# Performance work log

Measured on AMD Instinct MI355X. Metric: run time of the kernel, lower is better.

Reference implementation:

```python
import jax, jax.numpy as jnp
import numpy as np

LN_EPS = 1e-5

def setup_inputs() -> dict:
    key = jax.random.key(0)
    ks = jax.random.split(key, 4)
    B, N, D, De = 4, 2048, 128, 8
    h = jax.random.normal(ks[0], (B, N, D), dtype=jnp.float32)
    e = jax.random.normal(ks[1], (B, N, N, De), dtype=jnp.float32)
    W_w = jax.random.normal(ks[2], (D, D), dtype=jnp.float32) * (1.0 / np.sqrt(D))
    W_b = jax.random.normal(ks[3], (D,), dtype=jnp.float32) * 0.02
    ln_g = jnp.ones((D,), dtype=jnp.float32)
    ln_b = jnp.zeros((D,), dtype=jnp.float32)
    return {"h": h, "e": e, "W_w": W_w, "W_b": W_b, "ln_g": ln_g, "ln_b": ln_b}

def _layernorm(x, g, b):
    mu = jnp.mean(x, axis=-1, keepdims=True)
    var = jnp.var(x, axis=-1, keepdims=True)
    return (x - mu) * jax.lax.rsqrt(var + LN_EPS) * g + b

def reference(h, e, W_w, W_b, ln_g, ln_b):
    # w_ij = softmax_j(||e_ij||)  -> [B, N, N]
    scores = jnp.linalg.norm(e, axis=-1)          # [B, N, N]
    w = jax.nn.softmax(scores, axis=2)            # softmax over neighbor dim j
    # agg_i = sum_j w_ij * h_j  (batched matmul instead of O(B N^2 D) broadcast)
    agg = jnp.einsum('bij,bjd->bid', w, h)        # [B, N, D]
    z = (h + agg) @ W_w.T + W_b                   # Linear
    h_new = jax.nn.relu(_layernorm(z, ln_g, ln_b)) + h
    return (h_new, e)
```

## Files before the change

kernel.cpp:

```cpp
#include <hip/hip_runtime.h>
#include <hip/hip_bf16.h>
#include <math.h>

constexpr int B  = 4;
constexpr int N  = 2048;
constexpr int D  = 128;
constexpr int De = 8;
constexpr int KS = 8;
constexpr float LN_EPS = 1e-5f;

__device__ inline ushort f2bf(float f) {
    uint u = __float_as_uint(f);
    return (ushort)((u + 0x7fffu + ((u >> 16) & 1u)) >> 16);
}

__global__ __launch_bounds__(256) void k_escore(const float* __restrict__ e,
                                                float* __restrict__ out_e,
                                                ushort* __restrict__ w16,
                                                long long total) {
    long long stride = (long long)gridDim.x * blockDim.x;
    for (long long idx = (long long)blockIdx.x * blockDim.x + threadIdx.x;
         idx < total; idx += stride) {
        const float4* src = reinterpret_cast<const float4*>(e + idx * De);
        float4 a  = src[0];
        float4 b4 = src[1];
        float4* dst = reinterpret_cast<float4*>(out_e + idx * De);
        dst[0] = a;
        dst[1] = b4;
        float ss = a.x * a.x + a.y * a.y + a.z * a.z + a.w * a.w
                 + b4.x * b4.x + b4.y * b4.y + b4.z * b4.z + b4.w * b4.w;
        w16[idx] = f2bf(__expf(sqrtf(ss)));
    }
}

__global__ __launch_bounds__(256) void k_rowsum(const ushort* __restrict__ w16,
                                                float* __restrict__ inv_rowsum) {
    __shared__ float red[4];
    long long row = blockIdx.x;
    int t = threadIdx.x;
    uint4 v = *reinterpret_cast<const uint4*>(w16 + row * (long long)N + t * 8);
    uint u[4] = {v.x, v.y, v.z, v.w};
    float s = 0.0f;
    #pragma unroll
    for (int q = 0; q < 4; ++q) {
        s += __uint_as_float(u[q] << 16);
        s += __uint_as_float(u[q] & 0xffff0000u);
    }
    #pragma unroll
    for (int off = 32; off > 0; off >>= 1) s += __shfl_xor(s, off);
    if ((t & 63) == 0) red[t >> 6] = s;
    __syncthreads();
    if (t == 0)
        inv_rowsum[row] = 1.0f / (red[0] + red[1] + red[2] + red[3]);
}

__global__ __launch_bounds__(256) void k_agg(const ushort* __restrict__ w16,
                                             const float* __restrict__ h,
                                             float* __restrict__ aggp) {
    constexpr int BM = 128;
    constexpr int BK = 32;
    constexpr int KC = N / KS;
    __shared__ ushort w_s[BK][BM + 8];
    __shared__ float  h_s[BK][D];

    int b  = blockIdx.y;
    int i0 = blockIdx.x * BM;
    int kbase = blockIdx.z * KC;
    int t  = threadIdx.x;
    int tc = t & 15;
    int tr = t >> 4;

    const ushort* wb = w16 + ((long long)b * N + i0) * N;
    const float*  hb = h + (long long)b * N * D;

    int sr = t >> 1, sh = t & 1;
    int hk = t >> 3, hc = (t & 7) * 16;

    float acc[8][8] = {};

    for (int k0 = kbase; k0 < kbase + KC; k0 += BK) {
        const uint4* wp = reinterpret_cast<const uint4*>(wb + (long long)sr * N + k0 + sh * 16);
        uint4 wa = wp[0];
        uint4 wc = wp[1];
        const float4* hp = reinterpret_cast<const float4*>(hb + (long long)(k0 + hk) * D + hc);
        float4 h0 = hp[0], h1 = hp[1], h2 = hp[2], h3 = hp[3];

        __syncthreads();

        uint u[8] = {wa.x, wa.y, wa.z, wa.w, wc.x, wc.y, wc.z, wc.w};
        #pragma unroll
        for (int q = 0; q < 8; ++q) {
            w_s[sh * 16 + 2 * q    ][sr] = (ushort)(u[q] & 0xffffu);
            w_s[sh * 16 + 2 * q + 1][sr] = (ushort)(u[q] >> 16);
        }
        float4* hsp = reinterpret_cast<float4*>(&h_s[hk][hc]);
        hsp[0] = h0; hsp[1] = h1; hsp[2] = h2; hsp[3] = h3;

        __syncthreads();

        #pragma unroll 8
        for (int kk = 0; kk < BK; ++kk) {
            uint4 wf  = *reinterpret_cast<const uint4*>(&w_s[kk][tr * 8]);
            float4 ha = *reinterpret_cast<const float4*>(&h_s[kk][tc * 8]);
            float4 hb4= *reinterpret_cast<const float4*>(&h_s[kk][tc * 8 + 4]);
            float wr[8];
            wr[0] = __uint_as_float(wf.x << 16); wr[1] = __uint_as_float(wf.x & 0xffff0000u);
            wr[2] = __uint_as_float(wf.y << 16); wr[3] = __uint_as_float(wf.y & 0xffff0000u);
            wr[4] = __uint_as_float(wf.z << 16); wr[5] = __uint_as_float(wf.z & 0xffff0000u);
            wr[6] = __uint_as_float(wf.w << 16); wr[7] = __uint_as_float(wf.w & 0xffff0000u);
            float hv[8] = {ha.x, ha.y, ha.z, ha.w, hb4.x, hb4.y, hb4.z, hb4.w};
            #pragma unroll
            for (int i = 0; i < 8; ++i)
                #pragma unroll
                for (int j = 0; j < 8; ++j)
                    acc[i][j] += wr[i] * hv[j];
        }
    }

    float* ap = aggp + (long long)blockIdx.z * B * N * D + ((long long)b * N + i0) * D;
    #pragma unroll
    for (int i = 0; i < 8; ++i) {
        float4 o0, o1;
        o0.x = acc[i][0]; o0.y = acc[i][1]; o0.z = acc[i][2]; o0.w = acc[i][3];
        o1.x = acc[i][4]; o1.y = acc[i][5]; o1.z = acc[i][6]; o1.w = acc[i][7];
        *reinterpret_cast<float4*>(ap + (long long)(tr * 8 + i) * D + tc * 8)     = o0;
        *reinterpret_cast<float4*>(ap + (long long)(tr * 8 + i) * D + tc * 8 + 4) = o1;
    }
}

__global__ __launch_bounds__(128) void k_out(const float* __restrict__ h,
                                             const float* __restrict__ aggp,
                                             const float* __restrict__ inv_rowsum,
                                             const float* __restrict__ Ww,
                                             const float* __restrict__ Wb,
                                             const float* __restrict__ ln_g,
                                             const float* __restrict__ ln_b,
                                             float* __restrict__ out) {
    __shared__ __align__(16) float x_s[D];
    __shared__ float red[4];
    constexpr long long BND = (long long)B * N * D;

    long long row = blockIdx.x;
    int d = threadIdx.x;

    float hv = h[row * D + d];
    float a = 0.0f;
    #pragma unroll
    for (int s = 0; s < KS; ++s)
        a += aggp[s * BND + row * D + d];
    a *= inv_rowsum[row];
    x_s[d] = hv + a;
    __syncthreads();

    const float4* wrow = reinterpret_cast<const float4*>(Ww + (long long)d * D);
    const float4* xv   = reinterpret_cast<const float4*>(x_s);
    float z = 0.0f;
    #pragma unroll
    for (int k = 0; k < D / 4; ++k) {
        float4 wv = wrow[k];
        float4 vv = xv[k];
        z += wv.x * vv.x + wv.y * vv.y + wv.z * vv.z + wv.w * vv.w;
    }
    z += Wb[d];

    float s = z;
    #pragma unroll
    for (int off = 32; off > 0; off >>= 1) s += __shfl_xor(s, off);
    if ((d & 63) == 0) red[d >> 6] = s;
    __syncthreads();
    float mu = (red[0] + red[1]) * (1.0f / (float)D);
    __syncthreads();

    float dev = z - mu;
    float s2 = dev * dev;
    #pragma unroll
    for (int off = 32; off > 0; off >>= 1) s2 += __shfl_xor(s2, off);
    if ((d & 63) == 0) red[d >> 6] = s2;
    __syncthreads();
    float var = (red[0] + red[1]) * (1.0f / (float)D);

    float y = dev * rsqrtf(var + LN_EPS) * ln_g[d] + ln_b[d];
    out[row * D + d] = fmaxf(y, 0.0f) + hv;
}

extern "C" void kernel_launch(void* const* d_in, const int* in_sizes, int n_in,
                              void* d_out, int out_size, void* d_ws, size_t ws_size,
                              hipStream_t stream) {
    const float* h    = (const float*)d_in[0];
    const float* e    = (const float*)d_in[1];
    const float* Ww   = (const float*)d_in[2];
    const float* Wb   = (const float*)d_in[3];
    const float* ln_g = (const float*)d_in[4];
    const float* ln_b = (const float*)d_in[5];

    float* out   = (float*)d_out;
    float* out_h = out;
    float* out_e = out + (size_t)B * N * D;

    ushort* w16 = (ushort*)d_ws;
    float*  aggp = (float*)(w16 + (size_t)B * N * N);
    float*  inv_rowsum = aggp + (size_t)KS * B * N * D;

    long long total = (long long)B * N * N;

    k_escore<<<4096, 256, 0, stream>>>(e, out_e, w16, total);
    k_rowsum<<<B * N, 256, 0, stream>>>(w16, inv_rowsum);
    dim3 g2(N / 128, B, KS);
    k_agg<<<g2, 256, 0, stream>>>(w16, h, aggp);
    k_out<<<B * N, 128, 0, stream>>>(h, aggp, inv_rowsum, Ww, Wb, ln_g, ln_b, out_h);
}
```

Baseline: 353.4 us.

## Use bf16 MFMA for aggregation with transposed bf16 h, widen escore per-thread work

Replaces the scalar FMA aggregation GEMM with MFMA 16x16x32 bf16 instructions. This needs a new kernel that casts h to bf16 and transposes it so both operands load K-contiguous into shared memory. The edge-score kernel now has each thread handle two edges with no grid-stride loop and packs two bf16 weights into one 32-bit store. h is now rounded to bf16 inside the aggregation, which adds precision error. The whole operation stays dominated by streaming the large e tensor.

```diff
diff --git a/kernel.cpp b/kernel.cpp
--- a/kernel.cpp
+++ b/kernel.cpp
@@ -9,6 +9,9 @@
 constexpr int KS = 8;
 constexpr float LN_EPS = 1e-5f;
 
+typedef __bf16 bf16x8 __attribute__((ext_vector_type(8)));
+typedef float  f32x4v __attribute__((ext_vector_type(4)));
+
 __device__ inline ushort f2bf(float f) {
     uint u = __float_as_uint(f);
     return (ushort)((u + 0x7fffu + ((u >> 16) & 1u)) >> 16);
@@ -16,21 +19,40 @@
 
 __global__ __launch_bounds__(256) void k_escore(const float* __restrict__ e,
                                                 float* __restrict__ out_e,
-                                                ushort* __restrict__ w16,
-                                                long long total) {
-    long long stride = (long long)gridDim.x * blockDim.x;
-    for (long long idx = (long long)blockIdx.x * blockDim.x + threadIdx.x;
-         idx < total; idx += stride) {
-        const float4* src = reinterpret_cast<const float4*>(e + idx * De);
-        float4 a  = src[0];
-        float4 b4 = src[1];
-        float4* dst = reinterpret_cast<float4*>(out_e + idx * De);
-        dst[0] = a;
-        dst[1] = b4;
-        float ss = a.x * a.x + a.y * a.y + a.z * a.z + a.w * a.w
-                 + b4.x * b4.x + b4.y * b4.y + b4.z * b4.z + b4.w * b4.w;
-        w16[idx] = f2bf(__expf(sqrtf(ss)));
-    }
+                                                uint* __restrict__ w16) {
+    long long tid = (long long)blockIdx.x * 256 + threadIdx.x;
+    const float4* src = reinterpret_cast<const float4*>(e + tid * 2 * De);
+    float4 a0 = src[0];
+    float4 a1 = src[1];
+    float4 a2 = src[2];
+    float4 a3 = src[3];
+    float4* dst = reinterpret_cast<float4*>(out_e + tid * 2 * De);
+    dst[0] = a0; dst[1] = a1; dst[2] = a2; dst[3] = a3;
+    float s0 = a0.x*a0.x + a0.y*a0.y + a0.z*a0.z + a0.w*a0.w
+             + a1.x*a1.x + a1.y*a1.y + a1.z*a1.z + a1.w*a1.w;
+    float s1 = a2.x*a2.x + a2.y*a2.y + a2.z*a2.z + a2.w*a2.w
+             + a3.x*a3.x + a3.y*a3.y + a3.z*a3.z + a3.w*a3.w;
+    uint p0 = f2bf(__expf(sqrtf(s0)));
+    uint p1 = f2bf(__expf(sqrtf(s1)));
+    w16[tid] = p0 | (p1 << 16);
+}
+
+__global__ __launch_bounds__(256) void k_hcast(const float* __restrict__ h,
+                                               ushort* __restrict__ hT16) {
+    __shared__ float tile[32][33];
+    int b  = blockIdx.z;
+    int n0 = blockIdx.x * 32, d0 = blockIdx.y * 32;
+    int t  = threadIdx.x;
+    int r = t >> 3, c = (t & 7) * 4;
+    float4 v = *reinterpret_cast<const float4*>(h + ((long long)b * N + n0 + r) * D + d0 + c);
+    tile[r][c] = v.x; tile[r][c + 1] = v.y; tile[r][c + 2] = v.z; tile[r][c + 3] = v.w;
+    __syncthreads();
+    ushort4 o;
+    o.x = f2bf(tile[c + 0][r]);
+    o.y = f2bf(tile[c + 1][r]);
+    o.z = f2bf(tile[c + 2][r]);
+    o.w = f2bf(tile[c + 3][r]);
+    *reinterpret_cast<ushort4*>(hT16 + ((long long)b * D + d0 + r) * N + n0 + c) = o;
 }
 
 __global__ __launch_bounds__(256) void k_rowsum(const ushort* __restrict__ w16,
@@ -55,77 +77,69 @@
 }
 
 __global__ __launch_bounds__(256) void k_agg(const ushort* __restrict__ w16,
-                                             const float* __restrict__ h,
+                                             const ushort* __restrict__ hT16,
                                              float* __restrict__ aggp) {
-    constexpr int BM = 128;
+    constexpr int BM = 64;
     constexpr int BK = 32;
     constexpr int KC = N / KS;
-    __shared__ ushort w_s[BK][BM + 8];
-    __shared__ float  h_s[BK][D];
+    __shared__ ushort A_s[BM][40];
+    __shared__ ushort B_s[D][40];
 
     int b  = blockIdx.y;
     int i0 = blockIdx.x * BM;
     int kbase = blockIdx.z * KC;
     int t  = threadIdx.x;
-    int tc = t & 15;
-    int tr = t >> 4;
-
-    const ushort* wb = w16 + ((long long)b * N + i0) * N;
-    const float*  hb = h + (long long)b * N * D;
-
-    int sr = t >> 1, sh = t & 1;
-    int hk = t >> 3, hc = (t & 7) * 16;
-
-    float acc[8][8] = {};
-
-    for (int k0 = kbase; k0 < kbase + KC; k0 += BK) {
-        const uint4* wp = reinterpret_cast<const uint4*>(wb + (long long)sr * N + k0 + sh * 16);
-        uint4 wa = wp[0];
-        uint4 wc = wp[1];
-        const float4* hp = reinterpret_cast<const float4*>(hb + (long long)(k0 + hk) * D + hc);
-        float4 h0 = hp[0], h1 = hp[1], h2 = hp[2], h3 = hp[3];
+    int wid = t >> 6, lane = t & 63;
+    int wr = wid >> 1, wc = wid & 1;
+    int lr = lane & 15, lk = (lane >> 4) * 8;
+
+    const ushort* wb = w16 + ((long long)b * N + i0) * N + kbase;
+    const ushort* hb = hT16 + (long long)b * D * N + kbase;
+
+    f32x4v acc[2][4] = {};
+
+    int ar = t >> 2, ac = (t & 3) * 8;
+    int q1 = t + 256;
+
+    for (int k0 = 0; k0 < KC; k0 += BK) {
+        uint4 av  = *reinterpret_cast<const uint4*>(wb + (long long)ar * N + k0 + ac);
+        uint4 bv0 = *reinterpret_cast<const uint4*>(hb + (long long)(t >> 2) * N + k0 + (t & 3) * 8);
+        uint4 bv1 = *reinterpret_cast<const uint4*>(hb + (long long)(q1 >> 2) * N + k0 + (q1 & 3) * 8);
 
         __syncthreads();
 
-        uint u[8] = {wa.x, wa.y, wa.z, wa.w, wc.x, wc.y, wc.z, wc.w};
-        #pragma unroll
-        for (int q = 0; q < 8; ++q) {
-            w_s[sh * 16 + 2 * q    ][sr] = (ushort)(u[q] & 0xffffu);
-            w_s[sh * 16 + 2 * q + 1][sr] = (ushort)(u[q] >> 16);
-        }
-        float4* hsp = reinterpret_cast<float4*>(&h_s[hk][hc]);
-        hsp[0] = h0; hsp[1] = h1; hsp[2] = h2; hsp[3] = h3;
+        *reinterpret_cast<uint4*>(&A_s[ar][ac]) = av;
+        *reinterpret_cast<uint4*>(&B_s[t >> 2][(t & 3) * 8]) = bv0;
+        *reinterpret_cast<uint4*>(&B_s[q1 >> 2][(q1 & 3) * 8]) = bv1;
 
         __syncthreads();
 
-        #pragma unroll 8
-        for (int kk = 0; kk < BK; ++kk) {
-            uint4 wf  = *reinterpret_cast<const uint4*>(&w_s[kk][tr * 8]);
-            float4 ha = *reinterpret_cast<const float4*>(&h_s[kk][tc * 8]);
-            float4 hb4= *reinterpret_cast<const float4*>(&h_s[kk][tc * 8 + 4]);
-            float wr[8];
-            wr[0] = __uint_as_float(wf.x << 16); wr[1] = __uint_as_float(wf.x & 0xffff0000u);
-            wr[2] = __uint_as_float(wf.y << 16); wr[3] = __uint_as_float(wf.y & 0xffff0000u);
-            wr[4] = __uint_as_float(wf.z << 16); wr[5] = __uint_as_float(wf.z & 0xffff0000u);
-            wr[6] = __uint_as_float(wf.w << 16); wr[7] = __uint_as_float(wf.w & 0xffff0000u);
-            float hv[8] = {ha.x, ha.y, ha.z, ha.w, hb4.x, hb4.y, hb4.z, hb4.w};
+        bf16x8 af[2], bfr[4];
+        #pragma unroll
+        for (int fm = 0; fm < 2; ++fm)
+            af[fm] = *reinterpret_cast<const bf16x8*>(&A_s[wr * 32 + fm * 16 + lr][lk]);
+        #pragma unroll
+        for (int fn = 0; fn < 4; ++fn)
+            bfr[fn] = *reinterpret_cast<const bf16x8*>(&B_s[wc * 64 + fn * 16 + lr][lk]);
+        #pragma unroll
+        for (int fm = 0; fm < 2; ++fm)
             #pragma unroll
-            for (int i = 0; i < 8; ++i)
-                #pragma unroll
-                for (int j = 0; j < 8; ++j)
-                    acc[i][j] += wr[i] * hv[j];
-        }
+            for (int fn = 0; fn < 4; ++fn)
+                acc[fm][fn] = __builtin_amdgcn_mfma_f32_16x16x32_bf16(
+                    af[fm], bfr[fn], acc[fm][fn], 0, 0, 0);
     }
 
     float* ap = aggp + (long long)blockIdx.z * B * N * D + ((long long)b * N + i0) * D;
     #pragma unroll
-    for (int i = 0; i < 8; ++i) {
-        float4 o0, o1;
-        o0.x = acc[i][0]; o0.y = acc[i][1]; o0.z = acc[i][2]; o0.w = acc[i][3];
-        o1.x = acc[i][4]; o1.y = acc[i][5]; o1.z = acc[i][6]; o1.w = acc[i][7];
-        *reinterpret_cast<float4*>(ap + (long long)(tr * 8 + i) * D + tc * 8)     = o0;
-        *reinterpret_cast<float4*>(ap + (long long)(tr * 8 + i) * D + tc * 8 + 4) = o1;
-    }
+    for (int fm = 0; fm < 2; ++fm)
+        #pragma unroll
+        for (int fn = 0; fn < 4; ++fn)
+            #pragma unroll
+            for (int r = 0; r < 4; ++r) {
+                int row = wr * 32 + fm * 16 + (lane >> 4) * 4 + r;
+                int col = wc * 64 + fn * 16 + lr;
+                ap[(long long)row * D + col] = acc[fm][fn][r];
+            }
 }
 
 __global__ __launch_bounds__(128) void k_out(const float* __restrict__ h,
@@ -197,15 +211,18 @@
     float* out_h = out;
     float* out_e = out + (size_t)B * N * D;
 
-    ushort* w16 = (ushort*)d_ws;
-    float*  aggp = (float*)(w16 + (size_t)B * N * N);
+    ushort* w16  = (ushort*)d_ws;
+    ushort* hT16 = w16 + (size_t)B * N * N;
+    float*  aggp = (float*)(hT16 + (size_t)B * D * N);
     float*  inv_rowsum = aggp + (size_t)KS * B * N * D;
 
-    long long total = (long long)B * N * N;
-
-    k_escore<<<4096, 256, 0, stream>>>(e, out_e, w16, total);
+    long long threads = (long long)B * N * N / 2;
+
+    k_escore<<<(int)(threads / 256), 256, 0, stream>>>(e, out_e, (uint*)w16);
+    dim3 gh(N / 32, D / 32, B);
+    k_hcast<<<gh, 256, 0, stream>>>(h, hT16);
     k_rowsum<<<B * N, 256, 0, stream>>>(w16, inv_rowsum);
-    dim3 g2(N / 128, B, KS);
-    k_agg<<<g2, 256, 0, stream>>>(w16, h, aggp);
+    dim3 g2(N / 64, B, KS);
+    k_agg<<<g2, 256, 0, stream>>>(w16, hT16, aggp);
     k_out<<<B * N, 128, 0, stream>>>(h, aggp, inv_rowsum, Ww, Wb, ln_g, ln_b, out_h);
 }
```

Measured after the change: 329.1 us. -6.9%, faster.
